# Kernel tuning notes

Measured on AMD Instinct MI355X. Metric: run time of the kernel, lower is better.

## Reference

```python
import jax, jax.numpy as jnp
import numpy as np

B, T, D = 2048, 200, 128
H1, H2 = 128, 64
MASK_PAD = -4294967295.0  # -2**32 + 1, as in the TF code


def prelu(x, alpha):
    return jnp.where(x > 0, x, alpha * x)


def setup_inputs() -> dict:
    key = jax.random.key(0)
    ks = jax.random.split(key, 12)
    query = jax.random.normal(ks[0], (B, D), dtype=jnp.float32)
    keyt = jax.random.normal(ks[1], (B, T, D), dtype=jnp.float32)
    val = jax.random.normal(ks[2], (B, T, D), dtype=jnp.float32)
    mask = jax.random.randint(ks[3], (B, T), 0, 2, dtype=jnp.int32)
    s = 0.05
    W0 = jax.random.normal(ks[4], (4 * D, H1), dtype=jnp.float32) * s
    b0 = jnp.zeros((H1,), dtype=jnp.float32)
    a0 = jnp.full((T, H1), 0.25, dtype=jnp.float32)  # Keras PReLU alpha: input_shape[1:]
    W1 = jax.random.normal(ks[5], (H1, H2), dtype=jnp.float32) * s
    b1 = jnp.zeros((H2,), dtype=jnp.float32)
    a1 = jnp.full((T, H2), 0.25, dtype=jnp.float32)
    Wout = jax.random.normal(ks[6], (H2, 1), dtype=jnp.float32) * s
    bout = jnp.zeros((1,), dtype=jnp.float32)
    return {"query": query, "key": keyt, "val": val, "mask": mask,
            "W0": W0, "b0": b0, "a0": a0, "W1": W1, "b1": b1, "a1": a1,
            "Wout": Wout, "bout": bout}


def reference(query, key, val, mask, W0, b0, a0, W1, b1, a1, Wout, bout):
    # tile query across history positions: [B, D] -> [B, T, D]
    q = jnp.broadcast_to(query[:, None, :], key.shape)
    # DIN feature interaction: [B, T, 4D]
    feat = jnp.concatenate([q, key, q - key, q * key], axis=-1)
    h = prelu(jnp.einsum('btf,fh->bth', feat, W0) + b0, a0)
    h = prelu(jnp.einsum('bth,hg->btg', h, W1) + b1, a1)
    logits = (jnp.einsum('btg,go->bto', h, Wout) + bout)[..., 0]  # [B, T]
    logits = jnp.where(mask == 0, MASK_PAD, logits)
    attn = jax.nn.softmax(logits, axis=-1)  # [B, T]
    # weighted sum over values: [B, D]
    return jnp.einsum('bt,btd->bd', attn, val)
```

## Files before the change

### kernel.cpp

```cpp
#include <hip/hip_runtime.h>
#include <cstdint>

#define BB 2048
#define TT 200
#define DD 128
#define H1 128
#define H2 64
#define MASK_PAD -4294967295.0f

typedef __attribute__((ext_vector_type(8))) short short8;
typedef __attribute__((ext_vector_type(4))) float floatx4;

#define ATTN_OFF 57344

static __device__ __forceinline__ unsigned short f2bf(float x) {
  union { float f; unsigned int u; } v; v.f = x;
  unsigned int r = v.u + 0x7FFF + ((v.u >> 16) & 1);
  return (unsigned short)(r >> 16);
}

__global__ void din_fold(const float* __restrict__ W0,
                         const float* __restrict__ W1,
                         float* __restrict__ ws) {
  int i = blockIdx.x * blockDim.x + threadIdx.x;
  if (i < 16384) {
    int d = i >> 7, h = i & 127;
    ws[i] = W0[d * 128 + h] + W0[(256 + d) * 128 + h];
  } else if (i < 32768) {
    int j = i - 16384; int h = j >> 7, d = j & 127;
    ws[16384 + j] = W0[(128 + d) * 128 + h] - W0[(256 + d) * 128 + h];
  } else if (i < 49152) {
    int j = i - 32768; int h = j >> 7, d = j & 127;
    ws[32768 + j] = W0[(384 + d) * 128 + h];
  } else if (i < 57344) {
    int j = i - 49152; int g = j >> 7, h = j & 127;
    ((unsigned short*)(ws + 49152))[j] = f2bf(W1[h * 64 + g]);
  }
}

__global__ __launch_bounds__(256, 2) void din_logits(
    const float* __restrict__ query, const float* __restrict__ key,
    const int* __restrict__ mask,
    const float* __restrict__ b0, const float* __restrict__ a0,
    const float* __restrict__ b1, const float* __restrict__ a1,
    const float* __restrict__ Wout, const float* __restrict__ bout,
    const float* __restrict__ ws, float* __restrict__ attn_out) {
  const int b = blockIdx.x;
  const int tid = threadIdx.x;
  const int w = tid >> 6;
  const int l = tid & 63;

  __shared__ unsigned short Wb[128 * 128];
  __shared__ unsigned short W1s[64 * 128];
  __shared__ unsigned short A2[4][16 * 128];
  __shared__ float qs[DD];
  __shared__ float qas[H1];
  __shared__ float logitsAll[208];
  __shared__ float red4[8];

  const float* Wqac = ws;
  const float* WkT  = ws + 16384;
  const float* WdT  = ws + 32768;
  const unsigned short* W1tb = (const unsigned short*)(ws + 49152);

  if (tid < DD) qs[tid] = query[(size_t)b * DD + tid];
  __syncthreads();

  #pragma unroll
  for (int j = 0; j < 16; ++j) {
    int flat = j * 1024 + tid * 4;
    int h = flat >> 7, d = flat & 127;
    float4 kv = *(const float4*)(WkT + flat);
    float4 dv = *(const float4*)(WdT + flat);
    ushort4 u;
    u.x = f2bf(kv.x + qs[d] * dv.x);
    u.y = f2bf(kv.y + qs[d + 1] * dv.y);
    u.z = f2bf(kv.z + qs[d + 2] * dv.z);
    u.w = f2bf(kv.w + qs[d + 3] * dv.w);
    *(ushort4*)((char*)Wb + h * 256 + ((d * 2) ^ ((h & 7) << 4))) = u;
  }
  #pragma unroll
  for (int j = 0; j < 8; ++j) {
    int flat = j * 1024 + tid * 4;
    int g = flat >> 7, h = flat & 127;
    ushort4 u = *(const ushort4*)(W1tb + flat);
    *(ushort4*)((char*)W1s + g * 256 + ((h * 2) ^ ((g & 7) << 4))) = u;
  }
  if (tid < H1) {
    float acc = b0[tid];
    const float* wq = Wqac + tid;
    #pragma unroll 8
    for (int d = 0; d < DD; ++d) acc += qs[d] * wq[d * 128];
    qas[tid] = acc;
  }
  __syncthreads();

  const int kgrp = l >> 4;
  const int lr = l & 15;
  char* a2b = (char*)A2[w];

  float b1v[4], wov[4];
  #pragma unroll
  for (int nt = 0; nt < 4; ++nt) {
    int g = nt * 16 + lr;
    b1v[nt] = b1[g]; wov[nt] = Wout[g];
  }
  const float bout0 = bout[0];

  float4 fa[8];
  int mt = w;
  {
    int trow = mt * 16 + lr; if (trow > 199) trow = 199;
    const float* ar = key + ((size_t)b * TT + trow) * DD + kgrp * 8;
    #pragma unroll
    for (int ks = 0; ks < 4; ++ks) {
      fa[2 * ks]     = *(const float4*)(ar + ks * 32);
      fa[2 * ks + 1] = *(const float4*)(ar + ks * 32 + 4);
    }
  }

  #pragma unroll 1
  while (mt < 13) {
    short8 af[4];
    #pragma unroll
    for (int ks = 0; ks < 4; ++ks) {
      float4 f0 = fa[2 * ks], f1 = fa[2 * ks + 1];
      short8 t;
      t[0] = (short)f2bf(f0.x); t[1] = (short)f2bf(f0.y);
      t[2] = (short)f2bf(f0.z); t[3] = (short)f2bf(f0.w);
      t[4] = (short)f2bf(f1.x); t[5] = (short)f2bf(f1.y);
      t[6] = (short)f2bf(f1.z); t[7] = (short)f2bf(f1.w);
      af[ks] = t;
    }
    int mtn = mt + 4;
    if (mtn < 13) {
      int trow = mtn * 16 + lr; if (trow > 199) trow = 199;
      const float* ar = key + ((size_t)b * TT + trow) * DD + kgrp * 8;
      #pragma unroll
      for (int ks = 0; ks < 4; ++ks) {
        fa[2 * ks]     = *(const float4*)(ar + ks * 32);
        fa[2 * ks + 1] = *(const float4*)(ar + ks * 32 + 4);
      }
    }
    float a0v[8][4], a1v[4][4];
    #pragma unroll
    for (int r = 0; r < 4; ++r) {
      int tg = mt * 16 + kgrp * 4 + r; if (tg > 199) tg = 199;
      #pragma unroll
      for (int nt = 0; nt < 8; ++nt)
        a0v[nt][r] = a0[tg * H1 + nt * 16 + lr];
      #pragma unroll
      for (int nt = 0; nt < 4; ++nt)
        a1v[nt][r] = a1[tg * H2 + nt * 16 + lr];
    }

    floatx4 acc1[8];
    #pragma unroll
    for (int nt = 0; nt < 8; ++nt) acc1[nt] = (floatx4)(0.0f);
    #pragma unroll
    for (int ks = 0; ks < 4; ++ks) {
      #pragma unroll
      for (int nt = 0; nt < 8; ++nt) {
        int h = nt * 16 + lr;
        short8 bf = *(const short8*)((const char*)Wb + h * 256 +
                                     ((ks * 64 + kgrp * 16) ^ ((h & 7) << 4)));
        acc1[nt] = __builtin_amdgcn_mfma_f32_16x16x32_bf16(af[ks], bf, acc1[nt], 0, 0, 0);
      }
    }
    #pragma unroll
    for (int nt = 0; nt < 8; ++nt) {
      int h = nt * 16 + lr;
      float qa = qas[h];
      #pragma unroll
      for (int r = 0; r < 4; ++r) {
        int t_loc = kgrp * 4 + r;
        float v = acc1[nt][r] + qa;
        float a = a0v[nt][r];
        v = v > 0.0f ? v : a * v;
        *(unsigned short*)(a2b + t_loc * 256 + ((h * 2) ^ ((t_loc & 7) << 4))) = f2bf(v);
      }
    }
    short8 a2f[4];
    #pragma unroll
    for (int ks = 0; ks < 4; ++ks) {
      a2f[ks] = *(const short8*)(a2b + lr * 256 +
                                 ((ks * 64 + kgrp * 16) ^ ((lr & 7) << 4)));
    }
    floatx4 acc2[4];
    #pragma unroll
    for (int nt = 0; nt < 4; ++nt) acc2[nt] = (floatx4)(0.0f);
    #pragma unroll
    for (int ks = 0; ks < 4; ++ks) {
      #pragma unroll
      for (int nt = 0; nt < 4; ++nt) {
        int g = nt * 16 + lr;
        short8 bf = *(const short8*)((const char*)W1s + g * 256 +
                                     ((ks * 64 + kgrp * 16) ^ ((g & 7) << 4)));
        acc2[nt] = __builtin_amdgcn_mfma_f32_16x16x32_bf16(a2f[ks], bf, acc2[nt], 0, 0, 0);
      }
    }
    float p[4] = {0.f, 0.f, 0.f, 0.f};
    #pragma unroll
    for (int nt = 0; nt < 4; ++nt) {
      #pragma unroll
      for (int r = 0; r < 4; ++r) {
        float x = acc2[nt][r] + b1v[nt];
        float a = a1v[nt][r];
        x = x > 0.0f ? x : a * x;
        p[r] += x * wov[nt];
      }
    }
    #pragma unroll
    for (int m = 1; m < 16; m <<= 1) {
      #pragma unroll
      for (int r = 0; r < 4; ++r) p[r] += __shfl_xor(p[r], m);
    }
    if (lr == 0) {
      #pragma unroll
      for (int r = 0; r < 4; ++r) {
        int tg = mt * 16 + kgrp * 4 + r;
        if (tg < TT) {
          int mk = mask[(size_t)b * TT + tg];
          logitsAll[tg] = (mk == 0) ? MASK_PAD : (bout0 + p[r]);
        }
      }
    }
    mt = mtn;
  }
  __syncthreads();

  float lv = (tid < TT) ? logitsAll[tid] : -INFINITY;
  {
    float m = lv;
    #pragma unroll
    for (int off = 32; off >= 1; off >>= 1) m = fmaxf(m, __shfl_xor(m, off));
    if (l == 0) red4[w] = m;
  }
  __syncthreads();
  float mx = fmaxf(fmaxf(red4[0], red4[1]), fmaxf(red4[2], red4[3]));
  float e = (tid < TT) ? __expf(lv - mx) : 0.0f;
  {
    float s = e;
    #pragma unroll
    for (int off = 32; off >= 1; off >>= 1) s += __shfl_xor(s, off);
    if (l == 0) red4[4 + w] = s;
  }
  __syncthreads();
  float denom = red4[4] + red4[5] + red4[6] + red4[7];
  float inv = 1.0f / denom;
  if (tid < TT) attn_out[(size_t)b * TT + tid] = e * inv;
}

__global__ __launch_bounds__(256) void din_pv(
    const float* __restrict__ val, const float* __restrict__ attn,
    float* __restrict__ out) {
  const int b = blockIdx.x;
  const int tid = threadIdx.x;
  __shared__ float eL[TT];
  __shared__ float red[8 * DD];

  if (tid < TT) eL[tid] = attn[(size_t)b * TT + tid];
  __syncthreads();

  const int group = tid >> 5;
  const int d4 = (tid & 31) * 4;
  const float* vb = val + (size_t)b * TT * DD;
  float4 acc4 = make_float4(0.f, 0.f, 0.f, 0.f);
  #pragma unroll 5
  for (int t = group * 25; t < group * 25 + 25; ++t) {
    float4 v = *(const float4*)(vb + (size_t)t * DD + d4);
    float wt = eL[t];
    acc4.x += wt * v.x; acc4.y += wt * v.y;
    acc4.z += wt * v.z; acc4.w += wt * v.w;
  }
  *(float4*)&red[group * DD + d4] = acc4;
  __syncthreads();
  if (tid < DD) {
    float s = 0.0f;
    #pragma unroll
    for (int g = 0; g < 8; ++g) s += red[g * DD + tid];
    out[(size_t)b * DD + tid] = s;
  }
}

extern "C" void kernel_launch(void* const* d_in, const int* in_sizes, int n_in,
                              void* d_out, int out_size, void* d_ws, size_t ws_size,
                              hipStream_t stream) {
  const float* query = (const float*)d_in[0];
  const float* key   = (const float*)d_in[1];
  const float* val   = (const float*)d_in[2];
  const int*   mask  = (const int*)d_in[3];
  const float* W0    = (const float*)d_in[4];
  const float* b0    = (const float*)d_in[5];
  const float* a0    = (const float*)d_in[6];
  const float* W1    = (const float*)d_in[7];
  const float* b1    = (const float*)d_in[8];
  const float* a1    = (const float*)d_in[9];
  const float* Wout  = (const float*)d_in[10];
  const float* bout  = (const float*)d_in[11];
  float* out = (float*)d_out;
  float* ws  = (float*)d_ws;
  float* attn = ws + ATTN_OFF;

  hipLaunchKernelGGL(din_fold, dim3(224), dim3(256), 0, stream, W0, W1, ws);
  hipLaunchKernelGGL(din_logits, dim3(BB), dim3(256), 0, stream,
                     query, key, mask, b0, a0, b1, a1, Wout, bout, ws, attn);
  hipLaunchKernelGGL(din_pv, dim3(BB), dim3(256), 0, stream, val, attn, out);
}
```

Measured before the change: 198.0 us.

## Split per-batch weight build and query projection into separate kernels, read weights from global

Moves the per-batch folded weight matrix construction (Wk + q*Wd in bf16) and the query projection into dedicated kernels that write to workspace, so the logits kernel reads B-fragments straight from global/L2 instead of staging them in shared memory. PReLU alphas are pre-transposed for vectorized loads. The query projection now seeds the MFMA accumulator, and masking plus softmax move into the PV kernel. This frees shared memory and removes prologue syncs in the logits kernel. The cost is about 64 MB of extra global writes and reads for the per-batch weight matrices, plus more kernel launches.

```diff
diff --git a/kernel.cpp b/kernel.cpp
--- a/kernel.cpp
+++ b/kernel.cpp
@@ -11,7 +11,15 @@
 typedef __attribute__((ext_vector_type(8))) short short8;
 typedef __attribute__((ext_vector_type(4))) float floatx4;
 
-#define ATTN_OFF 57344
+#define WS_WQAC   0
+#define WS_WKT    16384
+#define WS_WDT    32768
+#define WS_W1TB   49152
+#define WS_A0T    53248
+#define WS_A1T    78848
+#define WS_LOGITS 91648
+#define WS_QAS    501248
+#define WS_WBG    763392
 
 static __device__ __forceinline__ unsigned short f2bf(float x) {
   union { float f; unsigned int u; } v; v.f = x;
@@ -19,86 +27,84 @@
   return (unsigned short)(r >> 16);
 }
 
-__global__ void din_fold(const float* __restrict__ W0,
-                         const float* __restrict__ W1,
-                         float* __restrict__ ws) {
+__global__ __launch_bounds__(256) void din_fold(
+    const float* __restrict__ W0, const float* __restrict__ W1,
+    const float* __restrict__ a0, const float* __restrict__ a1,
+    float* __restrict__ ws) {
   int i = blockIdx.x * blockDim.x + threadIdx.x;
   if (i < 16384) {
     int d = i >> 7, h = i & 127;
-    ws[i] = W0[d * 128 + h] + W0[(256 + d) * 128 + h];
-  } else if (i < 32768) {
-    int j = i - 16384; int h = j >> 7, d = j & 127;
-    ws[16384 + j] = W0[(128 + d) * 128 + h] - W0[(256 + d) * 128 + h];
-  } else if (i < 49152) {
-    int j = i - 32768; int h = j >> 7, d = j & 127;
-    ws[32768 + j] = W0[(384 + d) * 128 + h];
-  } else if (i < 57344) {
-    int j = i - 49152; int g = j >> 7, h = j & 127;
-    ((unsigned short*)(ws + 49152))[j] = f2bf(W1[h * 64 + g]);
-  }
+    ws[WS_WQAC + i] = W0[d * 128 + h] + W0[(256 + d) * 128 + h];
+    ws[WS_WKT + (h * 128 + d)] = W0[(128 + d) * 128 + h] - W0[(256 + d) * 128 + h];
+    ws[WS_WDT + (h * 128 + d)] = W0[(384 + d) * 128 + h];
+  } else if (i < 24576) {
+    int j = i - 16384; int g = j >> 7, h = j & 127;
+    ((unsigned short*)(ws + WS_W1TB))[j] = f2bf(W1[h * 64 + g]);
+  } else if (i < 50176) {
+    int j = i - 24576; int h = j / 200, t = j % 200;
+    ws[WS_A0T + j] = a0[t * H1 + h];
+  } else if (i < 62976) {
+    int j = i - 50176; int g = j / 200, t = j % 200;
+    ws[WS_A1T + j] = a1[t * H2 + g];
+  }
+}
+
+__global__ __launch_bounds__(256) void din_wbuild(
+    const float* __restrict__ query, const float* __restrict__ ws,
+    unsigned short* __restrict__ wbg) {
+  int idx = blockIdx.x * 256 + threadIdx.x;
+  int b = idx >> 11;
+  int rem = idx & 2047;
+  int h = rem >> 4;
+  int d0 = (rem & 15) * 8;
+  const float* wk = ws + WS_WKT + h * 128 + d0;
+  const float* wd = ws + WS_WDT + h * 128 + d0;
+  const float* qp = query + (size_t)b * DD + d0;
+  short8 o;
+  #pragma unroll
+  for (int e = 0; e < 8; ++e) o[e] = (short)f2bf(wk[e] + qp[e] * wd[e]);
+  *(short8*)(wbg + (size_t)b * 16384 + h * 128 + d0) = o;
+}
+
+__global__ __launch_bounds__(128) void din_qa(
+    const float* __restrict__ query, const float* __restrict__ b0,
+    const float* __restrict__ ws, float* __restrict__ qas_g) {
+  const int b = blockIdx.x;
+  const int h = threadIdx.x;
+  __shared__ float qsh[DD];
+  qsh[h] = query[(size_t)b * DD + h];
+  __syncthreads();
+  float acc = b0[h];
+  const float* wq = ws + WS_WQAC + h;
+  #pragma unroll 8
+  for (int d = 0; d < DD; ++d) acc += qsh[d] * wq[d * 128];
+  qas_g[(size_t)b * H1 + h] = acc;
 }
 
 __global__ __launch_bounds__(256, 2) void din_logits(
-    const float* __restrict__ query, const float* __restrict__ key,
-    const int* __restrict__ mask,
-    const float* __restrict__ b0, const float* __restrict__ a0,
-    const float* __restrict__ b1, const float* __restrict__ a1,
-    const float* __restrict__ Wout, const float* __restrict__ bout,
-    const float* __restrict__ ws, float* __restrict__ attn_out) {
+    const float* __restrict__ key, const float* __restrict__ ws,
+    const unsigned short* __restrict__ wbg, const float* __restrict__ qas_g,
+    const float* __restrict__ b1, const float* __restrict__ Wout,
+    const float* __restrict__ bout, float* __restrict__ lgout_all) {
   const int b = blockIdx.x;
   const int tid = threadIdx.x;
   const int w = tid >> 6;
   const int l = tid & 63;
-
-  __shared__ unsigned short Wb[128 * 128];
-  __shared__ unsigned short W1s[64 * 128];
+  const int lr = l & 15;
+  const int kgrp = l >> 4;
+
   __shared__ unsigned short A2[4][16 * 128];
-  __shared__ float qs[DD];
-  __shared__ float qas[H1];
-  __shared__ float logitsAll[208];
-  __shared__ float red4[8];
-
-  const float* Wqac = ws;
-  const float* WkT  = ws + 16384;
-  const float* WdT  = ws + 32768;
-  const unsigned short* W1tb = (const unsigned short*)(ws + 49152);
-
-  if (tid < DD) qs[tid] = query[(size_t)b * DD + tid];
-  __syncthreads();
-
+
+  const unsigned short* wb = wbg + (size_t)b * 16384;
+  const unsigned short* w1 = (const unsigned short*)(ws + WS_W1TB);
+  const float* a0T = ws + WS_A0T;
+  const float* a1T = ws + WS_A1T;
+  float* lgout = lgout_all + (size_t)b * TT;
+  char* a2b = (char*)A2[w];
+
+  float qv[8];
   #pragma unroll
-  for (int j = 0; j < 16; ++j) {
-    int flat = j * 1024 + tid * 4;
-    int h = flat >> 7, d = flat & 127;
-    float4 kv = *(const float4*)(WkT + flat);
-    float4 dv = *(const float4*)(WdT + flat);
-    ushort4 u;
-    u.x = f2bf(kv.x + qs[d] * dv.x);
-    u.y = f2bf(kv.y + qs[d + 1] * dv.y);
-    u.z = f2bf(kv.z + qs[d + 2] * dv.z);
-    u.w = f2bf(kv.w + qs[d + 3] * dv.w);
-    *(ushort4*)((char*)Wb + h * 256 + ((d * 2) ^ ((h & 7) << 4))) = u;
-  }
-  #pragma unroll
-  for (int j = 0; j < 8; ++j) {
-    int flat = j * 1024 + tid * 4;
-    int g = flat >> 7, h = flat & 127;
-    ushort4 u = *(const ushort4*)(W1tb + flat);
-    *(ushort4*)((char*)W1s + g * 256 + ((h * 2) ^ ((g & 7) << 4))) = u;
-  }
-  if (tid < H1) {
-    float acc = b0[tid];
-    const float* wq = Wqac + tid;
-    #pragma unroll 8
-    for (int d = 0; d < DD; ++d) acc += qs[d] * wq[d * 128];
-    qas[tid] = acc;
-  }
-  __syncthreads();
-
-  const int kgrp = l >> 4;
-  const int lr = l & 15;
-  char* a2b = (char*)A2[w];
-
+  for (int nt = 0; nt < 8; ++nt) qv[nt] = qas_g[(size_t)b * H1 + nt * 16 + lr];
   float b1v[4], wov[4];
   #pragma unroll
   for (int nt = 0; nt < 4; ++nt) {
@@ -108,9 +114,8 @@
   const float bout0 = bout[0];
 
   float4 fa[8];
-  int mt = w;
   {
-    int trow = mt * 16 + lr; if (trow > 199) trow = 199;
+    int trow = w * 16 + lr; if (trow > 199) trow = 199;
     const float* ar = key + ((size_t)b * TT + trow) * DD + kgrp * 8;
     #pragma unroll
     for (int ks = 0; ks < 4; ++ks) {
@@ -120,7 +125,7 @@
   }
 
   #pragma unroll 1
-  while (mt < 13) {
+  for (int mt = w; mt < 13; mt += 4) {
     short8 af[4];
     #pragma unroll
     for (int ks = 0; ks < 4; ++ks) {
@@ -132,9 +137,8 @@
       t[6] = (short)f2bf(f1.z); t[7] = (short)f2bf(f1.w);
       af[ks] = t;
     }
-    int mtn = mt + 4;
-    if (mtn < 13) {
-      int trow = mtn * 16 + lr; if (trow > 199) trow = 199;
+    {
+      int trow = (mt + 4) * 16 + lr; if (trow > 199) trow = 199;
       const float* ar = key + ((size_t)b * TT + trow) * DD + kgrp * 8;
       #pragma unroll
       for (int ks = 0; ks < 4; ++ks) {
@@ -142,44 +146,38 @@
         fa[2 * ks + 1] = *(const float4*)(ar + ks * 32 + 4);
       }
     }
-    float a0v[8][4], a1v[4][4];
-    #pragma unroll
-    for (int r = 0; r < 4; ++r) {
-      int tg = mt * 16 + kgrp * 4 + r; if (tg > 199) tg = 199;
-      #pragma unroll
-      for (int nt = 0; nt < 8; ++nt)
-        a0v[nt][r] = a0[tg * H1 + nt * 16 + lr];
-      #pragma unroll
-      for (int nt = 0; nt < 4; ++nt)
-        a1v[nt][r] = a1[tg * H2 + nt * 16 + lr];
-    }
 
     floatx4 acc1[8];
     #pragma unroll
-    for (int nt = 0; nt < 8; ++nt) acc1[nt] = (floatx4)(0.0f);
+    for (int nt = 0; nt < 8; ++nt) {
+      acc1[nt][0] = qv[nt]; acc1[nt][1] = qv[nt];
+      acc1[nt][2] = qv[nt]; acc1[nt][3] = qv[nt];
+    }
     #pragma unroll
     for (int ks = 0; ks < 4; ++ks) {
       #pragma unroll
       for (int nt = 0; nt < 8; ++nt) {
-        int h = nt * 16 + lr;
-        short8 bf = *(const short8*)((const char*)Wb + h * 256 +
-                                     ((ks * 64 + kgrp * 16) ^ ((h & 7) << 4)));
+        short8 bf = *(const short8*)(wb + (nt * 16 + lr) * 128 + ks * 32 + kgrp * 8);
         acc1[nt] = __builtin_amdgcn_mfma_f32_16x16x32_bf16(af[ks], bf, acc1[nt], 0, 0, 0);
       }
     }
+
+    const int tbase = mt * 16 + kgrp * 4;
+    const int tb = tbase > 196 ? 196 : tbase;
     #pragma unroll
     for (int nt = 0; nt < 8; ++nt) {
       int h = nt * 16 + lr;
-      float qa = qas[h];
+      float4 a0q = *(const float4*)(a0T + h * 200 + tb);
       #pragma unroll
       for (int r = 0; r < 4; ++r) {
         int t_loc = kgrp * 4 + r;
-        float v = acc1[nt][r] + qa;
-        float a = a0v[nt][r];
+        float v = acc1[nt][r];
+        float a = ((const float*)&a0q)[r];
         v = v > 0.0f ? v : a * v;
         *(unsigned short*)(a2b + t_loc * 256 + ((h * 2) ^ ((t_loc & 7) << 4))) = f2bf(v);
       }
     }
+
     short8 a2f[4];
     #pragma unroll
     for (int ks = 0; ks < 4; ++ks) {
@@ -193,19 +191,20 @@
     for (int ks = 0; ks < 4; ++ks) {
       #pragma unroll
       for (int nt = 0; nt < 4; ++nt) {
-        int g = nt * 16 + lr;
-        short8 bf = *(const short8*)((const char*)W1s + g * 256 +
-                                     ((ks * 64 + kgrp * 16) ^ ((g & 7) << 4)));
+        short8 bf = *(const short8*)(w1 + (nt * 16 + lr) * 128 + ks * 32 + kgrp * 8);
         acc2[nt] = __builtin_amdgcn_mfma_f32_16x16x32_bf16(a2f[ks], bf, acc2[nt], 0, 0, 0);
       }
     }
+
     float p[4] = {0.f, 0.f, 0.f, 0.f};
     #pragma unroll
     for (int nt = 0; nt < 4; ++nt) {
+      int g = nt * 16 + lr;
+      float4 a1q = *(const float4*)(a1T + g * 200 + tb);
       #pragma unroll
       for (int r = 0; r < 4; ++r) {
         float x = acc2[nt][r] + b1v[nt];
-        float a = a1v[nt][r];
+        float a = ((const float*)&a1q)[r];
         x = x > 0.0f ? x : a * x;
         p[r] += x * wov[nt];
       }
@@ -218,18 +217,30 @@
     if (lr == 0) {
       #pragma unroll
       for (int r = 0; r < 4; ++r) {
-        int tg = mt * 16 + kgrp * 4 + r;
-        if (tg < TT) {
-          int mk = mask[(size_t)b * TT + tg];
-          logitsAll[tg] = (mk == 0) ? MASK_PAD : (bout0 + p[r]);
-        }
-      }
-    }
-    mt = mtn;
-  }
-  __syncthreads();
-
-  float lv = (tid < TT) ? logitsAll[tid] : -INFINITY;
+        int tg = tbase + r;
+        if (tg < TT) lgout[tg] = bout0 + p[r];
+      }
+    }
+  }
+}
+
+__global__ __launch_bounds__(256) void din_pv(
+    const float* __restrict__ val, const int* __restrict__ mask,
+    const float* __restrict__ logits, float* __restrict__ out) {
+  const int b = blockIdx.x;
+  const int tid = threadIdx.x;
+  const int w = tid >> 6;
+  const int l = tid & 63;
+  __shared__ float eL[TT];
+  __shared__ float red4[8];
+  __shared__ float red[8 * DD];
+
+  float lv = -INFINITY;
+  if (tid < TT) {
+    float lg = logits[(size_t)b * TT + tid];
+    int mk = mask[(size_t)b * TT + tid];
+    lv = (mk == 0) ? MASK_PAD : lg;
+  }
   {
     float m = lv;
     #pragma unroll
@@ -246,20 +257,8 @@
     if (l == 0) red4[4 + w] = s;
   }
   __syncthreads();
-  float denom = red4[4] + red4[5] + red4[6] + red4[7];
-  float inv = 1.0f / denom;
-  if (tid < TT) attn_out[(size_t)b * TT + tid] = e * inv;
-}
-
-__global__ __launch_bounds__(256) void din_pv(
-    const float* __restrict__ val, const float* __restrict__ attn,
-    float* __restrict__ out) {
-  const int b = blockIdx.x;
-  const int tid = threadIdx.x;
-  __shared__ float eL[TT];
-  __shared__ float red[8 * DD];
-
-  if (tid < TT) eL[tid] = attn[(size_t)b * TT + tid];
+  float inv = 1.0f / (red4[4] + red4[5] + red4[6] + red4[7]);
+  if (tid < TT) eL[tid] = e * inv;
   __syncthreads();
 
   const int group = tid >> 5;
@@ -300,10 +299,14 @@
   const float* bout  = (const float*)d_in[11];
   float* out = (float*)d_out;
   float* ws  = (float*)d_ws;
-  float* attn = ws + ATTN_OFF;
-
-  hipLaunchKernelGGL(din_fold, dim3(224), dim3(256), 0, stream, W0, W1, ws);
+  unsigned short* wbg = (unsigned short*)(ws + WS_WBG);
+  float* qas_g  = ws + WS_QAS;
+  float* logits = ws + WS_LOGITS;
+
+  hipLaunchKernelGGL(din_fold, dim3(246), dim3(256), 0, stream, W0, W1, a0, a1, ws);
+  hipLaunchKernelGGL(din_wbuild, dim3(16384), dim3(256), 0, stream, query, ws, wbg);
+  hipLaunchKernelGGL(din_qa, dim3(BB), dim3(128), 0, stream, query, b0, ws, qas_g);
   hipLaunchKernelGGL(din_logits, dim3(BB), dim3(256), 0, stream,
-                     query, key, mask, b0, a0, b1, a1, Wout, bout, ws, attn);
-  hipLaunchKernelGGL(din_pv, dim3(BB), dim3(256), 0, stream, val, attn, out);
-}
+                     key, ws, wbg, qas_g, b1, Wout, bout, logits);
+  hipLaunchKernelGGL(din_pv, dim3(BB), dim3(256), 0, stream, val, mask, logits, out);
+}
```

Measured after the change: 428.4 us. 116% more time.
